# Kernel tuning notes

Measured on AMD Instinct MI355X. Metric: run time of the kernel, lower is better.

## Reference

```python
import jax, jax.numpy as jnp
import numpy as np

B = 4096
D_FULL, D_T1, D_T2 = 1024, 512, 512
N_SPEC, N_SHARED = 4, 4
HID, OUT = 512, 256


def _expert_params(key, n_experts, d_in):
    k1, k2, k3, k4 = jax.random.split(key, 4)
    s1 = 1.0 / np.sqrt(d_in)
    s2 = 1.0 / np.sqrt(HID)
    return {
        'W1': jax.random.uniform(k1, (n_experts, d_in, HID), jnp.float32, -s1, s1),
        'b1': jax.random.uniform(k2, (n_experts, HID), jnp.float32, -s1, s1),
        'W2': jax.random.uniform(k3, (n_experts, HID, OUT), jnp.float32, -s2, s2),
        'b2': jax.random.uniform(k4, (n_experts, OUT), jnp.float32, -s2, s2),
    }


def setup_inputs() -> dict:
    key = jax.random.key(0)
    ks = jax.random.split(key, 12)
    x_full = jax.random.normal(ks[0], (B, D_FULL), jnp.float32)
    x_task1 = jax.random.normal(ks[1], (B, D_T1), jnp.float32)
    x_task2 = jax.random.normal(ks[2], (B, D_T2), jnp.float32)
    ps = _expert_params(ks[3], N_SHARED, D_FULL)
    p1 = _expert_params(ks[4], N_SPEC, D_T1)
    p2 = _expert_params(ks[5], N_SPEC, D_T2)
    sg = 1.0 / np.sqrt(D_FULL)
    s1 = 1.0 / np.sqrt(D_T1)
    s2 = 1.0 / np.sqrt(D_T2)
    return {
        'x_full': x_full, 'x_task1': x_task1, 'x_task2': x_task2,
        'sh_W1': ps['W1'], 'sh_b1': ps['b1'], 'sh_W2': ps['W2'], 'sh_b2': ps['b2'],
        't1_W1': p1['W1'], 't1_b1': p1['b1'], 't1_W2': p1['W2'], 't1_b2': p1['b2'],
        't2_W1': p2['W1'], 't2_b1': p2['b1'], 't2_W2': p2['W2'], 't2_b2': p2['b2'],
        'gsh_W': jax.random.uniform(ks[6], (D_FULL, 2 * N_SPEC + N_SHARED), jnp.float32, -sg, sg),
        'gsh_b': jax.random.uniform(ks[7], (2 * N_SPEC + N_SHARED,), jnp.float32, -sg, sg),
        'g1_W': jax.random.uniform(ks[8], (D_T1, N_SPEC + N_SHARED), jnp.float32, -s1, s1),
        'g1_b': jax.random.uniform(ks[9], (N_SPEC + N_SHARED,), jnp.float32, -s1, s1),
        'g2_W': jax.random.uniform(ks[10], (D_T2, N_SPEC + N_SHARED), jnp.float32, -s2, s2),
        'g2_b': jax.random.uniform(ks[11], (N_SPEC + N_SHARED,), jnp.float32, -s2, s2),
    }


def _experts(x, W1, b1, W2, b2):
    # x: [B, D]; W1: [E, D, H] -> out [E, B, OUT]
    h = jax.nn.relu(jnp.einsum('bd,edh->ebh', x, W1) + b1[:, None, :])
    return jax.nn.relu(jnp.einsum('ebh,eho->ebo', h, W2) + b2[:, None, :])


def reference(x_full, x_task1, x_task2,
              sh_W1, sh_b1, sh_W2, sh_b2,
              t1_W1, t1_b1, t1_W2, t1_b2,
              t2_W1, t2_b1, t2_W2, t2_b2,
              gsh_W, gsh_b, g1_W, g1_b, g2_W, g2_b):
    eo_shared = _experts(x_full, sh_W1, sh_b1, sh_W2, sh_b2)    # [Es, B, OUT]
    eo_t1 = _experts(x_task1, t1_W1, t1_b1, t1_W2, t1_b2)       # [Et, B, OUT]
    eo_t2 = _experts(x_task2, t2_W1, t2_b1, t2_W2, t2_b2)       # [Et, B, OUT]

    g1 = jax.nn.softmax(x_task1 @ g1_W + g1_b, axis=1)          # [B, Et+Es]
    out1 = jnp.einsum('ebc,be->bc', jnp.concatenate([eo_t1, eo_shared], axis=0), g1)

    g2 = jax.nn.softmax(x_task2 @ g2_W + g2_b, axis=1)
    out2 = jnp.einsum('ebc,be->bc', jnp.concatenate([eo_t2, eo_shared], axis=0), g2)

    gsh = jax.nn.softmax(x_full @ gsh_W + gsh_b, axis=1)        # [B, 2Et+Es]
    out_sh = jnp.einsum('ebc,be->bc', jnp.concatenate([eo_t1, eo_t2, eo_shared], axis=0), gsh)

    return (out_sh, out1, out2)
```

## Files before the change

kernel.cpp:

```cpp
#include <hip/hip_runtime.h>

typedef unsigned short u16;
typedef __attribute__((ext_vector_type(8))) short short8;
typedef __attribute__((ext_vector_type(4))) float f32x4;

#define GL2LDS16(src, dst) __builtin_amdgcn_global_load_lds( \
    (const __attribute__((address_space(1))) void*)(src),    \
    (__attribute__((address_space(3))) void*)(dst), 16, 0, 0)

__device__ __forceinline__ u16 f2bf(float f) {
  union { float f; unsigned u; } v; v.f = f;
  unsigned r = v.u + 0x7fffu + ((v.u >> 16) & 1u);
  return (u16)(r >> 16);
}
__device__ __forceinline__ float bf2f(u16 h) {
  union { unsigned u; float f; } v; v.u = ((unsigned)h) << 16; return v.f;
}

__global__ void k_gates_cvt(const float* __restrict__ xf, const float* __restrict__ x1,
                            const float* __restrict__ x2,
                            const float* __restrict__ gshW, const float* __restrict__ gshB,
                            const float* __restrict__ g1W, const float* __restrict__ g1B,
                            const float* __restrict__ g2W, const float* __restrict__ g2B,
                            u16* __restrict__ xfb, u16* __restrict__ x1b, u16* __restrict__ x2b,
                            float* __restrict__ gsh, float* __restrict__ g1o,
                            float* __restrict__ g2o) {
  const int b = blockIdx.x, lane = threadIdx.x;
  float s[12];
#pragma unroll
  for (int j = 0; j < 12; ++j) s[j] = 0.f;
  {
    const float* xr = xf + (size_t)b * 1024;
    u16* xw = xfb + (size_t)b * 1024;
    for (int k = lane; k < 1024; k += 64) {
      float v = xr[k];
      xw[k] = f2bf(v);
      const float* wr = gshW + (size_t)k * 12;
#pragma unroll
      for (int j = 0; j < 12; ++j) s[j] += v * wr[j];
    }
  }
  float u[8], w[8];
#pragma unroll
  for (int j = 0; j < 8; ++j) { u[j] = 0.f; w[j] = 0.f; }
  {
    const float* xr1 = x1 + (size_t)b * 512;
    const float* xr2 = x2 + (size_t)b * 512;
    u16* xw1 = x1b + (size_t)b * 512;
    u16* xw2 = x2b + (size_t)b * 512;
    for (int k = lane; k < 512; k += 64) {
      float v1 = xr1[k], v2 = xr2[k];
      xw1[k] = f2bf(v1); xw2[k] = f2bf(v2);
      const float* w1r = g1W + (size_t)k * 8;
      const float* w2r = g2W + (size_t)k * 8;
#pragma unroll
      for (int j = 0; j < 8; ++j) { u[j] += v1 * w1r[j]; w[j] += v2 * w2r[j]; }
    }
  }
#pragma unroll
  for (int off = 32; off >= 1; off >>= 1) {
#pragma unroll
    for (int j = 0; j < 12; ++j) s[j] += __shfl_xor(s[j], off, 64);
#pragma unroll
    for (int j = 0; j < 8; ++j) { u[j] += __shfl_xor(u[j], off, 64); w[j] += __shfl_xor(w[j], off, 64); }
  }
  if (lane == 0) {
    float m = -1e30f, tot = 0.f;
#pragma unroll
    for (int j = 0; j < 12; ++j) { s[j] += gshB[j]; m = fmaxf(m, s[j]); }
#pragma unroll
    for (int j = 0; j < 12; ++j) { s[j] = __expf(s[j] - m); tot += s[j]; }
    float inv = 1.f / tot;
#pragma unroll
    for (int j = 0; j < 12; ++j) gsh[(size_t)b * 12 + j] = s[j] * inv;
    m = -1e30f; tot = 0.f;
#pragma unroll
    for (int j = 0; j < 8; ++j) { u[j] += g1B[j]; m = fmaxf(m, u[j]); }
#pragma unroll
    for (int j = 0; j < 8; ++j) { u[j] = __expf(u[j] - m); tot += u[j]; }
    inv = 1.f / tot;
#pragma unroll
    for (int j = 0; j < 8; ++j) g1o[(size_t)b * 8 + j] = u[j] * inv;
    m = -1e30f; tot = 0.f;
#pragma unroll
    for (int j = 0; j < 8; ++j) { w[j] += g2B[j]; m = fmaxf(m, w[j]); }
#pragma unroll
    for (int j = 0; j < 8; ++j) { w[j] = __expf(w[j] - m); tot += w[j]; }
    inv = 1.f / tot;
#pragma unroll
    for (int j = 0; j < 8; ++j) g2o[(size_t)b * 8 + j] = w[j] * inv;
  }
}

struct TD { const float* src; u16* dst; int lgTps; int lgNtx; int R; int C; int tileBase; };
struct TArgs { TD d[6]; };

__global__ void k_transpose_all(TArgs ta) {
  __shared__ float tile[32][33];
  const int x = blockIdx.x;
  int di = 0;
#pragma unroll
  for (int i = 1; i < 6; ++i)
    if (x >= ta.d[i].tileBase) di = i;
  TD d = ta.d[di];
  const int local = x - d.tileBase;
  const int slice = local >> d.lgTps;
  const int ti = local & ((1 << d.lgTps) - 1);
  const int tx = ti & ((1 << d.lgNtx) - 1);
  const int ty = ti >> d.lgNtx;
  const float* src = d.src + (size_t)slice * d.R * d.C;
  u16* dst = d.dst + (size_t)slice * d.R * d.C;
  const int c0 = tx * 32, r0 = ty * 32;
  const int ttx = threadIdx.x, tty = threadIdx.y;
#pragma unroll
  for (int i = tty; i < 32; i += 8)
    tile[i][ttx] = src[(size_t)(r0 + i) * d.C + (c0 + ttx)];
  __syncthreads();
#pragma unroll
  for (int i = tty; i < 32; i += 8)
    dst[(size_t)(c0 + i) * d.R + (r0 + ttx)] = f2bf(tile[ttx][i]);
}

struct GemmDesc {
  const u16* A;
  const u16* BT;
  const float* bias;
  u16* C;
  int K;
  int N;
  int T;
};
struct GemmArgs { GemmDesc d[12]; };

#define BARR __builtin_amdgcn_s_barrier()
#define WAITL0                                                   \
  {                                                              \
    asm volatile("s_waitcnt lgkmcnt(0)" ::: "memory");           \
    __builtin_amdgcn_sched_barrier(0);                           \
  }
#define WAITV0 asm volatile("s_waitcnt vmcnt(0)" ::: "memory")

__global__ __launch_bounds__(512, 4) void k_gemm128(GemmArgs args) {
  __shared__ __align__(16) u16 As[2 * 128 * 32];
  __shared__ __align__(16) u16 Bs[2 * 256 * 32];

  GemmDesc g = args.d[blockIdx.y];
  const int K = g.K, N = g.N, T = g.T;
  const int ntN = N >> 8;
  const int bx = blockIdx.x;
  const int nt = bx & (ntN - 1);
  const int bt = (ntN == 2) ? (bx >> 1) : bx;
  const int row0 = bt << 7;
  const int col0 = nt << 8;

  const int tid = threadIdx.x;
  const int lane = tid & 63;
  const int wid = tid >> 6;
  const int wm = wid & 1;
  const int wn = wid >> 1;
  const int lrow = lane & 15;
  const int lkq = lane >> 4;

  const int csw = (lkq ^ (lrow & 3)) * 16;
  int aoff[4], boff[4];
#pragma unroll
  for (int mi = 0; mi < 4; ++mi) aoff[mi] = (wm * 64 + mi * 16 + lrow) * 64 + csw;
#pragma unroll
  for (int ni = 0; ni < 4; ++ni) boff[ni] = (wn * 64 + ni * 16 + lrow) * 64 + csw;

  const int ar = tid >> 2;
  const int acs = (tid & 3) ^ (ar & 3);
  const u16* aSrc = g.A + (size_t)(row0 + ar) * K + acs * 8;
  const int br0 = tid >> 2;
  const int bc0 = (tid & 3) ^ (br0 & 3);
  const u16* bSrc0 = g.BT + (size_t)(col0 + br0) * K + bc0 * 8;
  const int br1 = 128 + (tid >> 2);
  const int bc1 = (tid & 3) ^ (br1 & 3);
  const u16* bSrc1 = g.BT + (size_t)(col0 + br1) * K + bc1 * 8;

  auto STAGE = [&](int buf, int t) {
    GL2LDS16(aSrc + (size_t)t * 32, &As[buf * 4096 + tid * 8]);
    GL2LDS16(bSrc0 + (size_t)t * 32, &Bs[buf * 8192 + tid * 8]);
    GL2LDS16(bSrc1 + (size_t)t * 32, &Bs[buf * 8192 + 4096 + tid * 8]);
  };

  f32x4 acc[4][4];
#pragma unroll
  for (int m = 0; m < 4; ++m)
#pragma unroll
    for (int n = 0; n < 4; ++n)
      acc[m][n] = (f32x4){0.f, 0.f, 0.f, 0.f};

  STAGE(0, 0);
  WAITV0;
  BARR;

  for (int t = 0; t < T; ++t) {
    const int buf = t & 1;
    const char* Ab = (const char*)As + buf * 8192;
    const char* Bb = (const char*)Bs + buf * 16384;
    short8 a0, a1, b[4];
#pragma unroll
    for (int ni = 0; ni < 4; ++ni) b[ni] = *(const short8*)(Bb + boff[ni]);
    a0 = *(const short8*)(Ab + aoff[0]);
    a1 = *(const short8*)(Ab + aoff[1]);
    if (t + 1 < T) STAGE(buf ^ 1, t + 1);
    WAITL0;
    __builtin_amdgcn_s_setprio(1);
#pragma unroll
    for (int ni = 0; ni < 4; ++ni) {
      acc[0][ni] = __builtin_amdgcn_mfma_f32_16x16x32_bf16(a0, b[ni], acc[0][ni], 0, 0, 0);
      acc[1][ni] = __builtin_amdgcn_mfma_f32_16x16x32_bf16(a1, b[ni], acc[1][ni], 0, 0, 0);
    }
    __builtin_amdgcn_s_setprio(0);
    a0 = *(const short8*)(Ab + aoff[2]);
    a1 = *(const short8*)(Ab + aoff[3]);
    WAITL0;
    __builtin_amdgcn_s_setprio(1);
#pragma unroll
    for (int ni = 0; ni < 4; ++ni) {
      acc[2][ni] = __builtin_amdgcn_mfma_f32_16x16x32_bf16(a0, b[ni], acc[2][ni], 0, 0, 0);
      acc[3][ni] = __builtin_amdgcn_mfma_f32_16x16x32_bf16(a1, b[ni], acc[3][ni], 0, 0, 0);
    }
    __builtin_amdgcn_s_setprio(0);
    WAITV0;
    BARR;
  }

#pragma unroll
  for (int ni = 0; ni < 4; ++ni) {
    const int gc = col0 + wn * 64 + ni * 16 + lrow;
    const float bv = g.bias[gc];
#pragma unroll
    for (int mi = 0; mi < 4; ++mi) {
      const int gr = row0 + wm * 64 + mi * 16 + lkq * 4;
#pragma unroll
      for (int j = 0; j < 4; ++j) {
        float o = fmaxf(acc[mi][ni][j] + bv, 0.f);
        g.C[(size_t)(gr + j) * N + gc] = f2bf(o);
      }
    }
  }
}

__global__ void k_reduce(const u16* __restrict__ OutB, const float* __restrict__ gsh,
                         const float* __restrict__ g1, const float* __restrict__ g2,
                         float* __restrict__ out) {
  int t = blockIdx.x * 256 + threadIdx.x;
  int b = t >> 5;
  int c0 = (t & 31) << 3;
  float wsh[12], w1[8], w2[8];
#pragma unroll
  for (int j = 0; j < 12; ++j) wsh[j] = gsh[(size_t)b * 12 + j];
#pragma unroll
  for (int j = 0; j < 8; ++j) { w1[j] = g1[(size_t)b * 8 + j]; w2[j] = g2[(size_t)b * 8 + j]; }
  float ash[8] = {0, 0, 0, 0, 0, 0, 0, 0};
  float a1[8] = {0, 0, 0, 0, 0, 0, 0, 0};
  float a2[8] = {0, 0, 0, 0, 0, 0, 0, 0};
#pragma unroll
  for (int e = 0; e < 12; ++e) {
    short8 v = *(const short8*)&OutB[((size_t)e * 4096 + b) * 256 + c0];
    float f[8];
#pragma unroll
    for (int i = 0; i < 8; ++i) f[i] = bf2f((u16)v[i]);
#pragma unroll
    for (int i = 0; i < 8; ++i) ash[i] += wsh[e] * f[i];
    if (e < 4) {
#pragma unroll
      for (int i = 0; i < 8; ++i) a1[i] += w1[e] * f[i];
    } else if (e < 8) {
#pragma unroll
      for (int i = 0; i < 8; ++i) a2[i] += w2[e - 4] * f[i];
    } else {
#pragma unroll
      for (int i = 0; i < 8; ++i) a1[i] += w1[e - 4] * f[i];
#pragma unroll
      for (int i = 0; i < 8; ++i) a2[i] += w2[e - 4] * f[i];
    }
  }
  size_t base = (size_t)b * 256 + c0;
  float4* o;
  o = (float4*)(out + base);
  o[0] = make_float4(ash[0], ash[1], ash[2], ash[3]);
  o[1] = make_float4(ash[4], ash[5], ash[6], ash[7]);
  o = (float4*)(out + 4096ull * 256 + base);
  o[0] = make_float4(a1[0], a1[1], a1[2], a1[3]);
  o[1] = make_float4(a1[4], a1[5], a1[6], a1[7]);
  o = (float4*)(out + 2ull * 4096 * 256 + base);
  o[0] = make_float4(a2[0], a2[1], a2[2], a2[3]);
  o[1] = make_float4(a2[4], a2[5], a2[6], a2[7]);
}

extern "C" void kernel_launch(void* const* d_in, const int* in_sizes, int n_in,
                              void* d_out, int out_size, void* d_ws, size_t ws_size,
                              hipStream_t stream) {
  const float* x_full = (const float*)d_in[0];
  const float* x_t1 = (const float*)d_in[1];
  const float* x_t2 = (const float*)d_in[2];
  const float* sh_W1 = (const float*)d_in[3];
  const float* sh_b1 = (const float*)d_in[4];
  const float* sh_W2 = (const float*)d_in[5];
  const float* sh_b2 = (const float*)d_in[6];
  const float* t1_W1 = (const float*)d_in[7];
  const float* t1_b1 = (const float*)d_in[8];
  const float* t1_W2 = (const float*)d_in[9];
  const float* t1_b2 = (const float*)d_in[10];
  const float* t2_W1 = (const float*)d_in[11];
  const float* t2_b1 = (const float*)d_in[12];
  const float* t2_W2 = (const float*)d_in[13];
  const float* t2_b2 = (const float*)d_in[14];
  const float* gsh_W = (const float*)d_in[15];
  const float* gsh_b = (const float*)d_in[16];
  const float* g1_W = (const float*)d_in[17];
  const float* g1_b = (const float*)d_in[18];
  const float* g2_W = (const float*)d_in[19];
  const float* g2_b = (const float*)d_in[20];

  char* ws = (char*)d_ws;
  size_t off = 0;
  auto alloc = [&](size_t bytes) -> void* {
    void* p = ws + off;
    off += (bytes + 255) & ~(size_t)255;
    return p;
  };
  u16* xf_b = (u16*)alloc(4096ull * 1024 * 2);
  u16* x1_b = (u16*)alloc(4096ull * 512 * 2);
  u16* x2_b = (u16*)alloc(4096ull * 512 * 2);
  u16* w1t_t1 = (u16*)alloc(4ull * 512 * 512 * 2);
  u16* w1t_t2 = (u16*)alloc(4ull * 512 * 512 * 2);
  u16* w1t_sh = (u16*)alloc(4ull * 512 * 1024 * 2);
  u16* w2t = (u16*)alloc(12ull * 256 * 512 * 2);
  u16* H = (u16*)alloc(12ull * 4096 * 512 * 2);
  u16* OutB = (u16*)alloc(12ull * 4096 * 256 * 2);
  float* gshv = (float*)alloc(4096ull * 12 * 4);
  float* g1v = (float*)alloc(4096ull * 8 * 4);
  float* g2v = (float*)alloc(4096ull * 8 * 4);

  k_gates_cvt<<<4096, 64, 0, stream>>>(x_full, x_t1, x_t2, gsh_W, gsh_b, g1_W, g1_b, g2_W, g2_b,
                                       xf_b, x1_b, x2_b, gshv, g1v, g2v);

  TArgs ta;
  ta.d[0] = TD{t1_W1, w1t_t1, 8, 4, 512, 512, 0};
  ta.d[1] = TD{t2_W1, w1t_t2, 8, 4, 512, 512, 1024};
  ta.d[2] = TD{sh_W1, w1t_sh, 9, 4, 1024, 512, 2048};
  ta.d[3] = TD{t1_W2, w2t, 7, 3, 512, 256, 4096};
  ta.d[4] = TD{t2_W2, w2t + 4ull * 256 * 512, 7, 3, 512, 256, 4608};
  ta.d[5] = TD{sh_W2, w2t + 8ull * 256 * 512, 7, 3, 512, 256, 5120};
  k_transpose_all<<<5632, dim3(32, 8), 0, stream>>>(ta);

  GemmArgs ga1;
  for (int e = 0; e < 4; ++e) {
    ga1.d[e] = GemmDesc{xf_b, w1t_sh + (size_t)e * 512 * 1024, sh_b1 + e * 512,
                        H + (size_t)(8 + e) * 4096 * 512, 1024, 512, 32};
    ga1.d[4 + e] = GemmDesc{x1_b, w1t_t1 + (size_t)e * 512 * 512, t1_b1 + e * 512,
                            H + (size_t)e * 4096 * 512, 512, 512, 16};
    ga1.d[8 + e] = GemmDesc{x2_b, w1t_t2 + (size_t)e * 512 * 512, t2_b1 + e * 512,
                            H + (size_t)(4 + e) * 4096 * 512, 512, 512, 16};
  }
  k_gemm128<<<dim3(64, 12), 512, 0, stream>>>(ga1);

  GemmArgs ga2;
  for (int e = 0; e < 12; ++e) {
    const float* bias = (e < 4) ? (t1_b2 + e * 256)
                      : (e < 8) ? (t2_b2 + (e - 4) * 256)
                                : (sh_b2 + (e - 8) * 256);
    ga2.d[e] = GemmDesc{H + (size_t)e * 4096 * 512, w2t + (size_t)e * 256 * 512, bias,
                        OutB + (size_t)e * 4096 * 256, 512, 256, 16};
  }
  k_gemm128<<<dim3(32, 12), 512, 0, stream>>>(ga2);

  k_reduce<<<512, 256, 0, stream>>>(OutB, gshv, g1v, g2v, (float*)d_out);
}
```

Before: 108.0 us.

## Vectorize gate kernel, retile second GEMM to 128-wide N, change LDS swizzle

The gate kernel now packs four batch rows per 256-thread block and uses float4 loads against pre-transposed gate weights, produced by a new small transpose kernel. This is meant to cut the strided scalar weight loads and the under-filled single-wave blocks. The GEMM is templated on its N tile: the second GEMM uses 128-wide tiles, which doubles its block count to fill more CUs. The LDS XOR swizzle also changes to key on (row>>1)&3 to reduce bank conflicts. The cost is one extra kernel launch, and the second GEMM does less compute per A-tile load.

```diff
diff --git a/kernel.cpp b/kernel.cpp
--- a/kernel.cpp
+++ b/kernel.cpp
@@ -17,44 +17,80 @@
   union { unsigned u; float f; } v; v.u = ((unsigned)h) << 16; return v.f;
 }
 
+__global__ void k_gateT(const float* __restrict__ gshW, const float* __restrict__ g1W,
+                        const float* __restrict__ g2W, float* __restrict__ gshWT,
+                        float* __restrict__ g1WT, float* __restrict__ g2WT) {
+  int idx = blockIdx.x * 256 + threadIdx.x;
+  if (idx < 12288) {
+    int j = idx >> 10, k = idx & 1023;
+    gshWT[j * 1024 + k] = gshW[k * 12 + j];
+  } else if (idx < 16384) {
+    int i2 = idx - 12288;
+    int j = i2 >> 9, k = i2 & 511;
+    g1WT[j * 512 + k] = g1W[k * 8 + j];
+  } else if (idx < 20480) {
+    int i2 = idx - 16384;
+    int j = i2 >> 9, k = i2 & 511;
+    g2WT[j * 512 + k] = g2W[k * 8 + j];
+  }
+}
+
 __global__ void k_gates_cvt(const float* __restrict__ xf, const float* __restrict__ x1,
                             const float* __restrict__ x2,
-                            const float* __restrict__ gshW, const float* __restrict__ gshB,
-                            const float* __restrict__ g1W, const float* __restrict__ g1B,
-                            const float* __restrict__ g2W, const float* __restrict__ g2B,
+                            const float* __restrict__ gshWT, const float* __restrict__ gshB,
+                            const float* __restrict__ g1WT, const float* __restrict__ g1B,
+                            const float* __restrict__ g2WT, const float* __restrict__ g2B,
                             u16* __restrict__ xfb, u16* __restrict__ x1b, u16* __restrict__ x2b,
                             float* __restrict__ gsh, float* __restrict__ g1o,
                             float* __restrict__ g2o) {
-  const int b = blockIdx.x, lane = threadIdx.x;
+  const int b = blockIdx.x * 4 + (threadIdx.x >> 6);
+  const int lane = threadIdx.x & 63;
   float s[12];
 #pragma unroll
   for (int j = 0; j < 12; ++j) s[j] = 0.f;
   {
-    const float* xr = xf + (size_t)b * 1024;
-    u16* xw = xfb + (size_t)b * 1024;
-    for (int k = lane; k < 1024; k += 64) {
-      float v = xr[k];
-      xw[k] = f2bf(v);
-      const float* wr = gshW + (size_t)k * 12;
-#pragma unroll
-      for (int j = 0; j < 12; ++j) s[j] += v * wr[j];
+    const float4* x4 = (const float4*)(xf + (size_t)b * 1024);
+    uint2* xw = (uint2*)(xfb + (size_t)b * 1024);
+#pragma unroll
+    for (int i = 0; i < 4; ++i) {
+      const int kc = lane + 64 * i;
+      float4 xv = x4[kc];
+      uint2 pk;
+      pk.x = (unsigned)f2bf(xv.x) | ((unsigned)f2bf(xv.y) << 16);
+      pk.y = (unsigned)f2bf(xv.z) | ((unsigned)f2bf(xv.w) << 16);
+      xw[kc] = pk;
+#pragma unroll
+      for (int j = 0; j < 12; ++j) {
+        float4 wv = *(const float4*)(gshWT + j * 1024 + 4 * kc);
+        s[j] += xv.x * wv.x + xv.y * wv.y + xv.z * wv.z + xv.w * wv.w;
+      }
     }
   }
   float u[8], w[8];
 #pragma unroll
   for (int j = 0; j < 8; ++j) { u[j] = 0.f; w[j] = 0.f; }
   {
-    const float* xr1 = x1 + (size_t)b * 512;
-    const float* xr2 = x2 + (size_t)b * 512;
-    u16* xw1 = x1b + (size_t)b * 512;
-    u16* xw2 = x2b + (size_t)b * 512;
-    for (int k = lane; k < 512; k += 64) {
-      float v1 = xr1[k], v2 = xr2[k];
-      xw1[k] = f2bf(v1); xw2[k] = f2bf(v2);
-      const float* w1r = g1W + (size_t)k * 8;
-      const float* w2r = g2W + (size_t)k * 8;
-#pragma unroll
-      for (int j = 0; j < 8; ++j) { u[j] += v1 * w1r[j]; w[j] += v2 * w2r[j]; }
+    const float4* x41 = (const float4*)(x1 + (size_t)b * 512);
+    const float4* x42 = (const float4*)(x2 + (size_t)b * 512);
+    uint2* xw1 = (uint2*)(x1b + (size_t)b * 512);
+    uint2* xw2 = (uint2*)(x2b + (size_t)b * 512);
+#pragma unroll
+    for (int i = 0; i < 2; ++i) {
+      const int kc = lane + 64 * i;
+      float4 v1 = x41[kc], v2 = x42[kc];
+      uint2 p1, p2;
+      p1.x = (unsigned)f2bf(v1.x) | ((unsigned)f2bf(v1.y) << 16);
+      p1.y = (unsigned)f2bf(v1.z) | ((unsigned)f2bf(v1.w) << 16);
+      p2.x = (unsigned)f2bf(v2.x) | ((unsigned)f2bf(v2.y) << 16);
+      p2.y = (unsigned)f2bf(v2.z) | ((unsigned)f2bf(v2.w) << 16);
+      xw1[kc] = p1; xw2[kc] = p2;
+#pragma unroll
+      for (int j = 0; j < 8; ++j) {
+        float4 w1v = *(const float4*)(g1WT + j * 512 + 4 * kc);
+        float4 w2v = *(const float4*)(g2WT + j * 512 + 4 * kc);
+        u[j] += v1.x * w1v.x + v1.y * w1v.y + v1.z * w1v.z + v1.w * w1v.w;
+        w[j] += v2.x * w2v.x + v2.y * w2v.y + v2.z * w2v.z + v2.w * w2v.w;
+      }
     }
   }
 #pragma unroll
@@ -140,18 +176,19 @@
   }
 #define WAITV0 asm volatile("s_waitcnt vmcnt(0)" ::: "memory")
 
-__global__ __launch_bounds__(512, 4) void k_gemm128(GemmArgs args) {
+template <int BN>
+__global__ __launch_bounds__(512, 4) void k_gemm(GemmArgs args) {
+  constexpr int NI = BN / 64;
   __shared__ __align__(16) u16 As[2 * 128 * 32];
-  __shared__ __align__(16) u16 Bs[2 * 256 * 32];
+  __shared__ __align__(16) u16 Bs[2 * BN * 32];
 
   GemmDesc g = args.d[blockIdx.y];
   const int K = g.K, N = g.N, T = g.T;
-  const int ntN = N >> 8;
   const int bx = blockIdx.x;
-  const int nt = bx & (ntN - 1);
-  const int bt = (ntN == 2) ? (bx >> 1) : bx;
+  const int nt = bx & 1;
+  const int bt = bx >> 1;
   const int row0 = bt << 7;
-  const int col0 = nt << 8;
+  const int col0 = nt * BN;
 
   const int tid = threadIdx.x;
   const int lane = tid & 63;
@@ -161,34 +198,35 @@
   const int lrow = lane & 15;
   const int lkq = lane >> 4;
 
-  const int csw = (lkq ^ (lrow & 3)) * 16;
-  int aoff[4], boff[4];
+  const int csw = (lkq ^ ((lrow >> 1) & 3)) * 16;
+  int aoff[4], boff[NI];
 #pragma unroll
   for (int mi = 0; mi < 4; ++mi) aoff[mi] = (wm * 64 + mi * 16 + lrow) * 64 + csw;
 #pragma unroll
-  for (int ni = 0; ni < 4; ++ni) boff[ni] = (wn * 64 + ni * 16 + lrow) * 64 + csw;
+  for (int ni = 0; ni < NI; ++ni) boff[ni] = (wn * (BN / 4) + ni * 16 + lrow) * 64 + csw;
 
   const int ar = tid >> 2;
-  const int acs = (tid & 3) ^ (ar & 3);
+  const int acs = (tid & 3) ^ ((ar >> 1) & 3);
   const u16* aSrc = g.A + (size_t)(row0 + ar) * K + acs * 8;
   const int br0 = tid >> 2;
-  const int bc0 = (tid & 3) ^ (br0 & 3);
+  const int bc0 = (tid & 3) ^ ((br0 >> 1) & 3);
   const u16* bSrc0 = g.BT + (size_t)(col0 + br0) * K + bc0 * 8;
   const int br1 = 128 + (tid >> 2);
-  const int bc1 = (tid & 3) ^ (br1 & 3);
+  const int bc1 = (tid & 3) ^ ((br1 >> 1) & 3);
   const u16* bSrc1 = g.BT + (size_t)(col0 + br1) * K + bc1 * 8;
 
   auto STAGE = [&](int buf, int t) {
     GL2LDS16(aSrc + (size_t)t * 32, &As[buf * 4096 + tid * 8]);
-    GL2LDS16(bSrc0 + (size_t)t * 32, &Bs[buf * 8192 + tid * 8]);
-    GL2LDS16(bSrc1 + (size_t)t * 32, &Bs[buf * 8192 + 4096 + tid * 8]);
+    GL2LDS16(bSrc0 + (size_t)t * 32, &Bs[buf * (BN * 32) + tid * 8]);
+    if constexpr (BN == 256)
+      GL2LDS16(bSrc1 + (size_t)t * 32, &Bs[buf * (BN * 32) + 4096 + tid * 8]);
   };
 
-  f32x4 acc[4][4];
+  f32x4 acc[4][NI];
 #pragma unroll
   for (int m = 0; m < 4; ++m)
 #pragma unroll
-    for (int n = 0; n < 4; ++n)
+    for (int n = 0; n < NI; ++n)
       acc[m][n] = (f32x4){0.f, 0.f, 0.f, 0.f};
 
   STAGE(0, 0);
@@ -198,17 +236,17 @@
   for (int t = 0; t < T; ++t) {
     const int buf = t & 1;
     const char* Ab = (const char*)As + buf * 8192;
-    const char* Bb = (const char*)Bs + buf * 16384;
-    short8 a0, a1, b[4];
-#pragma unroll
-    for (int ni = 0; ni < 4; ++ni) b[ni] = *(const short8*)(Bb + boff[ni]);
+    const char* Bb = (const char*)Bs + buf * (BN * 64);
+    short8 a0, a1, b[NI];
+#pragma unroll
+    for (int ni = 0; ni < NI; ++ni) b[ni] = *(const short8*)(Bb + boff[ni]);
     a0 = *(const short8*)(Ab + aoff[0]);
     a1 = *(const short8*)(Ab + aoff[1]);
     if (t + 1 < T) STAGE(buf ^ 1, t + 1);
     WAITL0;
     __builtin_amdgcn_s_setprio(1);
 #pragma unroll
-    for (int ni = 0; ni < 4; ++ni) {
+    for (int ni = 0; ni < NI; ++ni) {
       acc[0][ni] = __builtin_amdgcn_mfma_f32_16x16x32_bf16(a0, b[ni], acc[0][ni], 0, 0, 0);
       acc[1][ni] = __builtin_amdgcn_mfma_f32_16x16x32_bf16(a1, b[ni], acc[1][ni], 0, 0, 0);
     }
@@ -218,7 +256,7 @@
     WAITL0;
     __builtin_amdgcn_s_setprio(1);
 #pragma unroll
-    for (int ni = 0; ni < 4; ++ni) {
+    for (int ni = 0; ni < NI; ++ni) {
       acc[2][ni] = __builtin_amdgcn_mfma_f32_16x16x32_bf16(a0, b[ni], acc[2][ni], 0, 0, 0);
       acc[3][ni] = __builtin_amdgcn_mfma_f32_16x16x32_bf16(a1, b[ni], acc[3][ni], 0, 0, 0);
     }
@@ -228,8 +266,8 @@
   }
 
 #pragma unroll
-  for (int ni = 0; ni < 4; ++ni) {
-    const int gc = col0 + wn * 64 + ni * 16 + lrow;
+  for (int ni = 0; ni < NI; ++ni) {
+    const int gc = col0 + wn * (BN / 4) + ni * 16 + lrow;
     const float bv = g.bias[gc];
 #pragma unroll
     for (int mi = 0; mi < 4; ++mi) {
@@ -335,9 +373,14 @@
   float* gshv = (float*)alloc(4096ull * 12 * 4);
   float* g1v = (float*)alloc(4096ull * 8 * 4);
   float* g2v = (float*)alloc(4096ull * 8 * 4);
-
-  k_gates_cvt<<<4096, 64, 0, stream>>>(x_full, x_t1, x_t2, gsh_W, gsh_b, g1_W, g1_b, g2_W, g2_b,
-                                       xf_b, x1_b, x2_b, gshv, g1v, g2v);
+  float* gshWT = (float*)alloc(12ull * 1024 * 4);
+  float* g1WT = (float*)alloc(8ull * 512 * 4);
+  float* g2WT = (float*)alloc(8ull * 512 * 4);
+
+  k_gateT<<<80, 256, 0, stream>>>(gsh_W, g1_W, g2_W, gshWT, g1WT, g2WT);
+
+  k_gates_cvt<<<1024, 256, 0, stream>>>(x_full, x_t1, x_t2, gshWT, gsh_b, g1WT, g1_b,
+                                        g2WT, g2_b, xf_b, x1_b, x2_b, gshv, g1v, g2v);
 
   TArgs ta;
   ta.d[0] = TD{t1_W1, w1t_t1, 8, 4, 512, 512, 0};
@@ -357,7 +400,7 @@
     ga1.d[8 + e] = GemmDesc{x2_b, w1t_t2 + (size_t)e * 512 * 512, t2_b1 + e * 512,
                             H + (size_t)(4 + e) * 4096 * 512, 512, 512, 16};
   }
-  k_gemm128<<<dim3(64, 12), 512, 0, stream>>>(ga1);
+  k_gemm<256><<<dim3(64, 12), 512, 0, stream>>>(ga1);
 
   GemmArgs ga2;
   for (int e = 0; e < 12; ++e) {
@@ -367,7 +410,7 @@
     ga2.d[e] = GemmDesc{H + (size_t)e * 4096 * 512, w2t + (size_t)e * 256 * 512, bias,
                         OutB + (size_t)e * 4096 * 256, 512, 256, 16};
   }
-  k_gemm128<<<dim3(32, 12), 512, 0, stream>>>(ga2);
+  k_gemm<128><<<dim3(64, 12), 512, 0, stream>>>(ga2);
 
   k_reduce<<<512, 256, 0, stream>>>(OutB, gshv, g1v, g2v, (float*)d_out);
 }
```

Measured after the change: 116.3 us. +7.7%, slower.
